# Optimization experiments

Measured on AMD Instinct MI355X. Metric: run time of the kernel, lower is better.

Reference implementation:

```python
import jax, jax.numpy as jnp
import numpy as np

THRESHOLD = 0.05

def binarize101(w, threshold):
    # Ternary quantization to {-1, 0, +1}: zero inside the dead-zone [-thr, thr].
    pos = (w > threshold).astype(w.dtype)
    neg = (w < -threshold).astype(w.dtype)
    return pos - neg

def setup_inputs() -> dict:
    key = jax.random.key(0)
    k1, k2, k3 = jax.random.split(key, 3)
    x = jax.random.normal(k1, (8192, 4096), dtype=jnp.float32)
    weight = jax.random.normal(k2, (4096, 4096), dtype=jnp.float32)
    bias = jax.random.normal(k3, (4096,), dtype=jnp.float32)
    return {"x": x, "weight": weight, "bias": bias}

def reference(x, weight, bias):
    wb = binarize101(weight, THRESHOLD)
    # F.linear: x @ wb.T + bias ; x: [N, in], weight: [out, in] -> [N, out]
    return jnp.einsum('ni,oi->no', x, wb) + bias
```

## Files before the change

kernel.cpp:

```cpp
#include <hip/hip_runtime.h>

typedef float floatx16 __attribute__((ext_vector_type(16)));
typedef __bf16 bf16x8 __attribute__((ext_vector_type(8)));
using u16 = unsigned short;
using u32 = unsigned int;

#define GLOBAL_AS __attribute__((address_space(1)))
#define LDS_AS    __attribute__((address_space(3)))

__device__ __forceinline__ u32 rne_bf16(float f) {
  u32 u = __float_as_uint(f);
  return (u + 0x7FFFu + ((u >> 16) & 1u)) >> 16;
}

__global__ __launch_bounds__(256) void cvt_x_perm(const float* __restrict__ x,
                                                  u16* __restrict__ xb, int K) {
  __shared__ u16 sm[16384];
  const int tid = threadIdx.x;
  const int Kt = K >> 6;
  const int pn = blockIdx.x / Kt, tt = blockIdx.x % Kt;
  const float* src = x + (size_t)pn * 256 * K + tt * 64;
#pragma unroll
  for (int j = 0; j < 16; ++j) {
    const int fc = j * 256 + tid;
    const int row = fc >> 4, kl4 = fc & 15;
    const float4 v = *(const float4*)(src + (size_t)row * K + kl4 * 4);
    uint2 o;
    o.x = rne_bf16(v.x) | (rne_bf16(v.y) << 16);
    o.y = rne_bf16(v.z) | (rne_bf16(v.w) << 16);
    const int gi = row >> 5, rowin = row & 31;
    const int ks = kl4 >> 2;
    const int lane = rowin + 32 * ((kl4 >> 1) & 1);
    const int e4 = (kl4 & 1) * 4;
    *(uint2*)(sm + gi * 2048 + ks * 512 + lane * 8 + e4) = o;
  }
  __syncthreads();
  u16* dst = xb + (size_t)pn * 256 * K + (size_t)tt * 16384;
#pragma unroll
  for (int j = 0; j < 8; ++j) {
    const int o = (j * 256 + tid) * 8;
    *(uint4*)(dst + o) = *(const uint4*)(sm + o);
  }
}

__global__ __launch_bounds__(256) void quant_w_perm(const float* __restrict__ w,
                                                    u16* __restrict__ wb, int K) {
  __shared__ u16 sm[16384];
  const int tid = threadIdx.x;
  const int Kt = K >> 6;
  const int pn = blockIdx.x / Kt, tt = blockIdx.x % Kt;
  const float* src = w + (size_t)pn * 256 * K + tt * 64;
#pragma unroll
  for (int j = 0; j < 16; ++j) {
    const int fc = j * 256 + tid;
    const int row = fc >> 4, kl4 = fc & 15;
    const float4 v = *(const float4*)(src + (size_t)row * K + kl4 * 4);
    float vv[4] = {v.x, v.y, v.z, v.w};
    u32 r[4];
#pragma unroll
    for (int e = 0; e < 4; ++e)
      r[e] = (vv[e] > 0.05f) ? 0x3F80u : ((vv[e] < -0.05f) ? 0xBF80u : 0u);
    uint2 o;
    o.x = r[0] | (r[1] << 16);
    o.y = r[2] | (r[3] << 16);
    const int gi = row >> 5, rowin = row & 31;
    const int ks = kl4 >> 2;
    const int lane = rowin + 32 * ((kl4 >> 1) & 1);
    const int e4 = (kl4 & 1) * 4;
    *(uint2*)(sm + gi * 2048 + ks * 512 + lane * 8 + e4) = o;
  }
  __syncthreads();
  u16* dst = wb + (size_t)pn * 256 * K + (size_t)tt * 16384;
#pragma unroll
  for (int j = 0; j < 8; ++j) {
    const int o = (j * 256 + tid) * 8;
    *(uint4*)(dst + o) = *(const uint4*)(sm + o);
  }
}

__global__ __launch_bounds__(512, 2) void gemm_bin_flow(
    const u16* __restrict__ Ap, const u16* __restrict__ Bp,
    const float* __restrict__ bias, float* __restrict__ C,
    int M, int N, int K) {
  __shared__ u16 lds[65536];

  const int tid = threadIdx.x;
  const int w = tid >> 6, l = tid & 63;
  const int wr = w >> 2, wc = w & 3;

  const int nbn = N >> 8;
  int wg = blockIdx.x;
  const int nwg = gridDim.x;
  if ((nwg & 7) == 0) wg = (wg & 7) * (nwg >> 3) + (wg >> 3);
  const int bm = wg / nbn, bn = wg % nbn;

  const int T = K >> 6;

  const u16* const Abase = Ap + (size_t)bm * ((size_t)K << 8) + tid * 8;
  const u16* const Bbase = Bp + (size_t)bn * ((size_t)K << 8) + tid * 8;

  const u16* const afp0 = lds + wr * 8192 + l * 8;
  const u16* const bfp0 = lds + 16384 + wc * 4096 + l * 8;

  floatx16 acc[4][2] = {};
  bf16x8 af[8], af2[8], bflo[4], bfhi[4];

#define GLOAD(gptr, u16off)                                                    \
  __builtin_amdgcn_global_load_lds((const GLOBAL_AS void*)(gptr),              \
                                   (LDS_AS void*)(lds + (u16off)), 16, 0, 0)
#define STAGE8(tt, bufdst)                                                     \
  {                                                                            \
    const size_t tb_ = (size_t)(tt) * 16384;                                   \
    GLOAD(Abase + tb_ + 0 * 4096, (bufdst) + 0 + tid * 8);                     \
    GLOAD(Abase + tb_ + 1 * 4096, (bufdst) + 4096 + tid * 8);                  \
    GLOAD(Abase + tb_ + 2 * 4096, (bufdst) + 8192 + tid * 8);                  \
    GLOAD(Abase + tb_ + 3 * 4096, (bufdst) + 12288 + tid * 8);                 \
    GLOAD(Bbase + tb_ + 0 * 4096, (bufdst) + 16384 + tid * 8);                 \
    GLOAD(Bbase + tb_ + 1 * 4096, (bufdst) + 20480 + tid * 8);                 \
    GLOAD(Bbase + tb_ + 2 * 4096, (bufdst) + 24576 + tid * 8);                 \
    GLOAD(Bbase + tb_ + 3 * 4096, (bufdst) + 28672 + tid * 8);                 \
  }

  STAGE8(0, 0)
  asm volatile("s_waitcnt vmcnt(0)" ::: "memory");
  __builtin_amdgcn_s_barrier();

  for (int t = 0; t < T; ++t) {
    const int bufc = (t & 1) << 15;
    const int bufo = bufc ^ 32768;
    const bool st1 = (t + 1 < T);

    if (st1) STAGE8(t + 1, bufo)

    const u16* afp = afp0 + bufc;
    const u16* bfp = bfp0 + bufc;

#pragma unroll
    for (int m = 0; m < 2; ++m)
#pragma unroll
      for (int ks = 0; ks < 4; ++ks)
        af[m * 4 + ks] = *(const bf16x8*)(afp + m * 2048 + ks * 512);
#pragma unroll
    for (int ks = 0; ks < 4; ++ks) bflo[ks] = *(const bf16x8*)(bfp + ks * 512);
#pragma unroll
    for (int ks = 0; ks < 4; ++ks) bfhi[ks] = *(const bf16x8*)(bfp + 2048 + ks * 512);

    asm volatile("s_waitcnt lgkmcnt(4)" ::: "memory");
    __builtin_amdgcn_sched_barrier(0);
    __builtin_amdgcn_s_setprio(1);
#pragma unroll
    for (int ks = 0; ks < 4; ++ks)
#pragma unroll
      for (int m = 0; m < 2; ++m)
        acc[m][0] = __builtin_amdgcn_mfma_f32_32x32x16_bf16(
            af[m * 4 + ks], bflo[ks], acc[m][0], 0, 0, 0);
    __builtin_amdgcn_s_setprio(0);

#pragma unroll
    for (int m = 0; m < 2; ++m)
#pragma unroll
      for (int ks = 0; ks < 4; ++ks)
        af2[m * 4 + ks] = *(const bf16x8*)(afp + 4096 + m * 2048 + ks * 512);

    asm volatile("s_waitcnt lgkmcnt(8)" ::: "memory");
    __builtin_amdgcn_sched_barrier(0);
    __builtin_amdgcn_s_setprio(1);
#pragma unroll
    for (int ks = 0; ks < 4; ++ks)
#pragma unroll
      for (int m = 0; m < 2; ++m)
        acc[m][1] = __builtin_amdgcn_mfma_f32_32x32x16_bf16(
            af[m * 4 + ks], bfhi[ks], acc[m][1], 0, 0, 0);
    __builtin_amdgcn_s_setprio(0);

    asm volatile("s_waitcnt lgkmcnt(0)" ::: "memory");
    __builtin_amdgcn_sched_barrier(0);
    __builtin_amdgcn_s_setprio(1);
#pragma unroll
    for (int ks = 0; ks < 4; ++ks)
#pragma unroll
      for (int m = 0; m < 2; ++m)
        acc[2 + m][0] = __builtin_amdgcn_mfma_f32_32x32x16_bf16(
            af2[m * 4 + ks], bflo[ks], acc[2 + m][0], 0, 0, 0);
#pragma unroll
    for (int ks = 0; ks < 4; ++ks)
#pragma unroll
      for (int m = 0; m < 2; ++m)
        acc[2 + m][1] = __builtin_amdgcn_mfma_f32_32x32x16_bf16(
            af2[m * 4 + ks], bfhi[ks], acc[2 + m][1], 0, 0, 0);
    __builtin_amdgcn_s_setprio(0);

    if (st1) {
      asm volatile("s_waitcnt vmcnt(0)" ::: "memory");
      __builtin_amdgcn_s_barrier();
    }
  }
#undef STAGE8
#undef GLOAD

  const int colq = l & 31;
  const int hi4 = (l >> 5) * 4;
#pragma unroll
  for (int m = 0; m < 4; ++m) {
    const int rowb = bm * 256 + wr * 128 + m * 32 + hi4;
#pragma unroll
    for (int n = 0; n < 2; ++n) {
      const int col = bn * 256 + wc * 64 + n * 32 + colq;
      const float bv = bias[col];
      float* cp = C + (size_t)rowb * N + col;
#pragma unroll
      for (int q = 0; q < 16; ++q) {
        const int dr = (q & 3) + 8 * (q >> 2);
        cp[(size_t)dr * N] = acc[m][n][q] + bv;
      }
    }
  }
}

__global__ void gemm_naive_kernel(const float* __restrict__ x, const float* __restrict__ wgt,
                                  const float* __restrict__ bias, float* __restrict__ out,
                                  int M, int N, int K) {
  long long idx = (long long)blockIdx.x * blockDim.x + threadIdx.x;
  if (idx >= (long long)M * N) return;
  int o = (int)(idx % N);
  int m = (int)(idx / N);
  const float* xr = x + (size_t)m * K;
  const float* wr = wgt + (size_t)o * K;
  float s = 0.f;
  for (int i = 0; i < K; ++i) {
    float wv = wr[i];
    float t = (wv > 0.05f) ? 1.f : ((wv < -0.05f) ? -1.f : 0.f);
    s = fmaf(xr[i], t, s);
  }
  out[idx] = s + bias[o];
}

extern "C" void kernel_launch(void* const* d_in, const int* in_sizes, int n_in,
                              void* d_out, int out_size, void* d_ws, size_t ws_size,
                              hipStream_t stream) {
  const float* x    = (const float*)d_in[0];
  const float* wgt  = (const float*)d_in[1];
  const float* bias = (const float*)d_in[2];
  float* out = (float*)d_out;

  const int N = in_sizes[2];
  const int K = in_sizes[1] / N;
  const int M = in_sizes[0] / K;

  const size_t need = ((size_t)M * K + (size_t)N * K) * sizeof(u16);
  if (ws_size >= need && (M % 256 == 0) && (N % 256 == 0) && (K % 64 == 0) && K >= 192) {
    u16* xb = (u16*)d_ws;
    u16* wb = xb + (size_t)M * K;
    const int Kt = K / 64;
    cvt_x_perm<<<(M / 256) * Kt, 256, 0, stream>>>(x, xb, K);
    quant_w_perm<<<(N / 256) * Kt, 256, 0, stream>>>(wgt, wb, K);
    const int grid = (M / 256) * (N / 256);
    gemm_bin_flow<<<grid, 512, 0, stream>>>(xb, wb, bias, out, M, N, K);
  } else {
    const long long total = (long long)M * N;
    gemm_naive_kernel<<<(unsigned)((total + 255) / 256), 256, 0, stream>>>(x, wgt, bias, out, M, N, K);
  }
}
```

Measured before the change: 290.5 us.

## Pack ternary weights to 2 bits and decode B fragments in registers

The weight quantizer now writes each ternary value as a 2-bit code, packed in a fragment-ordered layout, so the GEMM loads B straight from global memory into registers and decodes it to bf16 there. The B tile no longer goes through LDS, which halves LDS use, cuts B global traffic by 8x, and frees registers by reusing one A fragment array. The A staging is reorganised into split half-tile loads overlapped with compute using a two-tile-ahead schedule and an extra barrier. The costs are ALU work for decoding inside the main loop, uncoalesced 2-byte scattered writes in the pack kernel, and a stricter K requirement (multiple of 128).

Result: slower. 359.4 us (+23.7%).

```diff
diff --git a/kernel.cpp b/kernel.cpp
--- a/kernel.cpp
+++ b/kernel.cpp
@@ -43,46 +43,46 @@
   }
 }
 
-__global__ __launch_bounds__(256) void quant_w_perm(const float* __restrict__ w,
-                                                    u16* __restrict__ wb, int K) {
-  __shared__ u16 sm[16384];
-  const int tid = threadIdx.x;
+__global__ void quant_w_pack(const float* __restrict__ w, u16* __restrict__ wb,
+                             int K, int Kd8, int n8) {
+  int stride = gridDim.x * blockDim.x;
   const int Kt = K >> 6;
-  const int pn = blockIdx.x / Kt, tt = blockIdx.x % Kt;
-  const float* src = w + (size_t)pn * 256 * K + tt * 64;
-#pragma unroll
-  for (int j = 0; j < 16; ++j) {
-    const int fc = j * 256 + tid;
-    const int row = fc >> 4, kl4 = fc & 15;
-    const float4 v = *(const float4*)(src + (size_t)row * K + kl4 * 4);
-    float vv[4] = {v.x, v.y, v.z, v.w};
-    u32 r[4];
-#pragma unroll
-    for (int e = 0; e < 4; ++e)
-      r[e] = (vv[e] > 0.05f) ? 0x3F80u : ((vv[e] < -0.05f) ? 0xBF80u : 0u);
-    uint2 o;
-    o.x = r[0] | (r[1] << 16);
-    o.y = r[2] | (r[3] << 16);
-    const int gi = row >> 5, rowin = row & 31;
-    const int ks = kl4 >> 2;
-    const int lane = rowin + 32 * ((kl4 >> 1) & 1);
-    const int e4 = (kl4 & 1) * 4;
-    *(uint2*)(sm + gi * 2048 + ks * 512 + lane * 8 + e4) = o;
-  }
-  __syncthreads();
-  u16* dst = wb + (size_t)pn * 256 * K + (size_t)tt * 16384;
-#pragma unroll
-  for (int j = 0; j < 8; ++j) {
-    const int o = (j * 256 + tid) * 8;
-    *(uint4*)(dst + o) = *(const uint4*)(sm + o);
-  }
-}
-
-__global__ __launch_bounds__(512, 2) void gemm_bin_flow(
+  for (int i = blockIdx.x * blockDim.x + threadIdx.x; i < n8; i += stride) {
+    const int n = i / Kd8;
+    const int k = (i - n * Kd8) * 8;
+    const float4* p = (const float4*)(w + (size_t)n * K + k);
+    float4 a = p[0], b = p[1];
+    float v[8] = {a.x, a.y, a.z, a.w, b.x, b.y, b.z, b.w};
+    u32 pk = 0;
+#pragma unroll
+    for (int j = 0; j < 8; ++j) {
+      u32 c = (v[j] > 0.05f) ? 1u : ((v[j] < -0.05f) ? 3u : 0u);
+      pk |= c << (2 * j);
+    }
+    const int bnp = n >> 8, wc = (n >> 6) & 3, ng = (n >> 5) & 1, cc = n & 31;
+    const int t = k >> 6, ks = (k >> 4) & 3, h = (k >> 3) & 1;
+    const int f = ng * 4 + ks, l = cc + 32 * h;
+    wb[(size_t)((bnp * Kt + t) * 4 + wc) * 512 + l * 8 + f] = (u16)pk;
+  }
+}
+
+__device__ __forceinline__ bf16x8 dec_frag(u32 pkv) {
+  union { u32 w[4]; bf16x8 v; } u;
+#pragma unroll
+  for (int ii = 0; ii < 4; ++ii) {
+    u32 x = (pkv >> (4 * ii)) & 0xFu;
+    u32 lo = (x & 1u) * 0x3F80u | ((x & 2u) << 14);
+    u32 hi = ((x >> 2) & 1u) * 0x3F80u | ((x & 8u) << 12);
+    u.w[ii] = lo | (hi << 16);
+  }
+  return u.v;
+}
+
+__global__ __launch_bounds__(512, 2) void gemm_bin_breg(
     const u16* __restrict__ Ap, const u16* __restrict__ Bp,
     const float* __restrict__ bias, float* __restrict__ C,
     int M, int N, int K) {
-  __shared__ u16 lds[65536];
+  __shared__ u16 lds[32768];
 
   const int tid = threadIdx.x;
   const int w = tid >> 6, l = tid & 63;
@@ -95,107 +95,116 @@
   const int bm = wg / nbn, bn = wg % nbn;
 
   const int T = K >> 6;
+  const int Kt = T;
 
   const u16* const Abase = Ap + (size_t)bm * ((size_t)K << 8) + tid * 8;
-  const u16* const Bbase = Bp + (size_t)bn * ((size_t)K << 8) + tid * 8;
+  const u16* const pkp = Bp + (size_t)((size_t)bn * Kt * 4 + wc) * 512 + l * 8;
 
   const u16* const afp0 = lds + wr * 8192 + l * 8;
-  const u16* const bfp0 = lds + 16384 + wc * 4096 + l * 8;
 
   floatx16 acc[4][2] = {};
-  bf16x8 af[8], af2[8], bflo[4], bfhi[4];
+  bf16x8 af[8], bflo[4], bfhi[4];
+  uint4 pkA, pkB;
 
 #define GLOAD(gptr, u16off)                                                    \
   __builtin_amdgcn_global_load_lds((const GLOBAL_AS void*)(gptr),              \
                                    (LDS_AS void*)(lds + (u16off)), 16, 0, 0)
-#define STAGE8(tt, bufdst)                                                     \
+
+  pkA = *(const uint4*)(pkp);
+  GLOAD(Abase + 0 * 4096,      0 + tid * 8);
+  GLOAD(Abase + 1 * 4096,   4096 + tid * 8);
+  GLOAD(Abase + 2 * 4096,   8192 + tid * 8);
+  GLOAD(Abase + 3 * 4096,  12288 + tid * 8);
+  if (T > 1) {
+    GLOAD(Abase + 16384 + 0 * 4096, 16384 + 0 + tid * 8);
+    GLOAD(Abase + 16384 + 2 * 4096, 16384 + 8192 + tid * 8);
+    pkB = *(const uint4*)(pkp + 2048);
+  }
+  asm volatile("s_waitcnt vmcnt(3)" ::: "memory");
+  __builtin_amdgcn_s_barrier();
+
+#define TILE(t, PKX)                                                           \
   {                                                                            \
-    const size_t tb_ = (size_t)(tt) * 16384;                                   \
-    GLOAD(Abase + tb_ + 0 * 4096, (bufdst) + 0 + tid * 8);                     \
-    GLOAD(Abase + tb_ + 1 * 4096, (bufdst) + 4096 + tid * 8);                  \
-    GLOAD(Abase + tb_ + 2 * 4096, (bufdst) + 8192 + tid * 8);                  \
-    GLOAD(Abase + tb_ + 3 * 4096, (bufdst) + 12288 + tid * 8);                 \
-    GLOAD(Bbase + tb_ + 0 * 4096, (bufdst) + 16384 + tid * 8);                 \
-    GLOAD(Bbase + tb_ + 1 * 4096, (bufdst) + 20480 + tid * 8);                 \
-    GLOAD(Bbase + tb_ + 2 * 4096, (bufdst) + 24576 + tid * 8);                 \
-    GLOAD(Bbase + tb_ + 3 * 4096, (bufdst) + 28672 + tid * 8);                 \
-  }
-
-  STAGE8(0, 0)
-  asm volatile("s_waitcnt vmcnt(0)" ::: "memory");
-  __builtin_amdgcn_s_barrier();
-
-  for (int t = 0; t < T; ++t) {
-    const int bufc = (t & 1) << 15;
-    const int bufo = bufc ^ 32768;
-    const bool st1 = (t + 1 < T);
-
-    if (st1) STAGE8(t + 1, bufo)
-
-    const u16* afp = afp0 + bufc;
-    const u16* bfp = bfp0 + bufc;
-
-#pragma unroll
-    for (int m = 0; m < 2; ++m)
-#pragma unroll
-      for (int ks = 0; ks < 4; ++ks)
-        af[m * 4 + ks] = *(const bf16x8*)(afp + m * 2048 + ks * 512);
-#pragma unroll
-    for (int ks = 0; ks < 4; ++ks) bflo[ks] = *(const bf16x8*)(bfp + ks * 512);
-#pragma unroll
-    for (int ks = 0; ks < 4; ++ks) bfhi[ks] = *(const bf16x8*)(bfp + 2048 + ks * 512);
-
-    asm volatile("s_waitcnt lgkmcnt(4)" ::: "memory");
-    __builtin_amdgcn_sched_barrier(0);
-    __builtin_amdgcn_s_setprio(1);
-#pragma unroll
-    for (int ks = 0; ks < 4; ++ks)
-#pragma unroll
-      for (int m = 0; m < 2; ++m)
-        acc[m][0] = __builtin_amdgcn_mfma_f32_32x32x16_bf16(
-            af[m * 4 + ks], bflo[ks], acc[m][0], 0, 0, 0);
-    __builtin_amdgcn_s_setprio(0);
-
-#pragma unroll
-    for (int m = 0; m < 2; ++m)
-#pragma unroll
-      for (int ks = 0; ks < 4; ++ks)
-        af2[m * 4 + ks] = *(const bf16x8*)(afp + 4096 + m * 2048 + ks * 512);
-
-    asm volatile("s_waitcnt lgkmcnt(8)" ::: "memory");
-    __builtin_amdgcn_sched_barrier(0);
-    __builtin_amdgcn_s_setprio(1);
-#pragma unroll
-    for (int ks = 0; ks < 4; ++ks)
-#pragma unroll
-      for (int m = 0; m < 2; ++m)
-        acc[m][1] = __builtin_amdgcn_mfma_f32_32x32x16_bf16(
-            af[m * 4 + ks], bfhi[ks], acc[m][1], 0, 0, 0);
-    __builtin_amdgcn_s_setprio(0);
-
-    asm volatile("s_waitcnt lgkmcnt(0)" ::: "memory");
-    __builtin_amdgcn_sched_barrier(0);
-    __builtin_amdgcn_s_setprio(1);
-#pragma unroll
-    for (int ks = 0; ks < 4; ++ks)
-#pragma unroll
-      for (int m = 0; m < 2; ++m)
-        acc[2 + m][0] = __builtin_amdgcn_mfma_f32_32x32x16_bf16(
-            af2[m * 4 + ks], bflo[ks], acc[2 + m][0], 0, 0, 0);
-#pragma unroll
-    for (int ks = 0; ks < 4; ++ks)
-#pragma unroll
-      for (int m = 0; m < 2; ++m)
-        acc[2 + m][1] = __builtin_amdgcn_mfma_f32_32x32x16_bf16(
-            af2[m * 4 + ks], bfhi[ks], acc[2 + m][1], 0, 0, 0);
-    __builtin_amdgcn_s_setprio(0);
-
-    if (st1) {
-      asm volatile("s_waitcnt vmcnt(0)" ::: "memory");
-      __builtin_amdgcn_s_barrier();
-    }
-  }
-#undef STAGE8
+    const int bufc = ((t) & 1) << 14;                                          \
+    const int bufo = bufc ^ 16384;                                             \
+    const bool st1 = (t) + 1 < T;                                              \
+    const bool st2 = (t) + 2 < T;                                              \
+    const u16* afp = afp0 + bufc;                                              \
+           \
+    _Pragma("unroll")                                                          \
+    for (int m = 0; m < 2; ++m)                                                \
+      _Pragma("unroll")                                                        \
+      for (int ks = 0; ks < 4; ++ks)                                           \
+        af[m * 4 + ks] = *(const bf16x8*)(afp + m * 2048 + ks * 512);          \
+    if (st1) {                                                                 \
+      const size_t tb_ = (size_t)((t) + 1) * 16384;                            \
+      GLOAD(Abase + tb_ + 1 * 4096, bufo + 4096 + tid * 8);                    \
+      GLOAD(Abase + tb_ + 3 * 4096, bufo + 12288 + tid * 8);                   \
+    }                                                                          \
+    _Pragma("unroll")                                                          \
+    for (int ks = 0; ks < 4; ++ks) bflo[ks] = dec_frag((ks & 1) ? (((const u32*)&PKX)[ks >> 1] >> 16) : (((const u32*)&PKX)[ks >> 1] & 0xFFFFu)); \
+    asm volatile("s_waitcnt lgkmcnt(0)" ::: "memory");                         \
+    __builtin_amdgcn_sched_barrier(0);                                         \
+    __builtin_amdgcn_s_barrier();         \
+    __builtin_amdgcn_s_setprio(1);                                             \
+    _Pragma("unroll")                                                          \
+    for (int ks = 0; ks < 4; ++ks)                                             \
+      _Pragma("unroll")                                                        \
+      for (int m = 0; m < 2; ++m)                                              \
+        acc[m][0] = __builtin_amdgcn_mfma_f32_32x32x16_bf16(                   \
+            af[m * 4 + ks], bflo[ks], acc[m][0], 0, 0, 0);                     \
+    __builtin_amdgcn_s_setprio(0);                                             \
+                         \
+    if (st2) {                                                                 \
+      const size_t tb_ = (size_t)((t) + 2) * 16384;                            \
+      GLOAD(Abase + tb_ + 0 * 4096, bufc + 0 + tid * 8);                       \
+      GLOAD(Abase + tb_ + 2 * 4096, bufc + 8192 + tid * 8);                    \
+    }                                                                          \
+    _Pragma("unroll")                                                          \
+    for (int ks = 0; ks < 4; ++ks) bfhi[ks] = dec_frag((ks & 1) ? (((const u32*)&PKX)[2 + (ks >> 1)] >> 16) : (((const u32*)&PKX)[2 + (ks >> 1)] & 0xFFFFu)); \
+    __builtin_amdgcn_s_setprio(1);                                             \
+    _Pragma("unroll")                                                          \
+    for (int ks = 0; ks < 4; ++ks)                                             \
+      _Pragma("unroll")                                                        \
+      for (int m = 0; m < 2; ++m)                                              \
+        acc[m][1] = __builtin_amdgcn_mfma_f32_32x32x16_bf16(                   \
+            af[m * 4 + ks], bfhi[ks], acc[m][1], 0, 0, 0);                     \
+    __builtin_amdgcn_s_setprio(0);                                             \
+                                                  \
+    _Pragma("unroll")                                                          \
+    for (int m = 0; m < 2; ++m)                                                \
+      _Pragma("unroll")                                                        \
+      for (int ks = 0; ks < 4; ++ks)                                           \
+        af[m * 4 + ks] = *(const bf16x8*)(afp + 4096 + m * 2048 + ks * 512);   \
+    if (st2) PKX = *(const uint4*)(pkp + (size_t)((t) + 2) * 2048);            \
+    asm volatile("s_waitcnt lgkmcnt(0)" ::: "memory");                         \
+    __builtin_amdgcn_sched_barrier(0);                                         \
+    __builtin_amdgcn_s_setprio(1);                                             \
+    _Pragma("unroll")                                                          \
+    for (int ks = 0; ks < 4; ++ks)                                             \
+      _Pragma("unroll")                                                        \
+      for (int m = 0; m < 2; ++m)                                              \
+        acc[2 + m][0] = __builtin_amdgcn_mfma_f32_32x32x16_bf16(               \
+            af[m * 4 + ks], bflo[ks], acc[2 + m][0], 0, 0, 0);                 \
+    _Pragma("unroll")                                                          \
+    for (int ks = 0; ks < 4; ++ks)                                             \
+      _Pragma("unroll")                                                        \
+      for (int m = 0; m < 2; ++m)                                              \
+        acc[2 + m][1] = __builtin_amdgcn_mfma_f32_32x32x16_bf16(               \
+            af[m * 4 + ks], bfhi[ks], acc[2 + m][1], 0, 0, 0);                 \
+    __builtin_amdgcn_s_setprio(0);                                             \
+    if (st1) {                                                                 \
+      if (st2) asm volatile("s_waitcnt vmcnt(3)" ::: "memory");                \
+      else     asm volatile("s_waitcnt vmcnt(0)" ::: "memory");                \
+      __builtin_amdgcn_s_barrier();         \
+    }                                                                          \
+  }
+
+  for (int tt = 0; tt < T; tt += 2) {
+    TILE(tt,     pkA)
+    TILE(tt + 1, pkB)
+  }
+#undef TILE
 #undef GLOAD
 
   const int colq = l & 31;
@@ -247,15 +256,15 @@
   const int K = in_sizes[1] / N;
   const int M = in_sizes[0] / K;
 
-  const size_t need = ((size_t)M * K + (size_t)N * K) * sizeof(u16);
-  if (ws_size >= need && (M % 256 == 0) && (N % 256 == 0) && (K % 64 == 0) && K >= 192) {
+  const size_t need = (size_t)M * K * 2 + (size_t)N * K / 4;
+  if (ws_size >= need && (M % 256 == 0) && (N % 256 == 0) && (K % 128 == 0) && K >= 256) {
     u16* xb = (u16*)d_ws;
     u16* wb = xb + (size_t)M * K;
     const int Kt = K / 64;
     cvt_x_perm<<<(M / 256) * Kt, 256, 0, stream>>>(x, xb, K);
-    quant_w_perm<<<(N / 256) * Kt, 256, 0, stream>>>(wgt, wb, K);
+    quant_w_pack<<<2048, 256, 0, stream>>>(wgt, wb, K, K / 8, (N * K) / 8);
     const int grid = (M / 256) * (N / 256);
-    gemm_bin_flow<<<grid, 512, 0, stream>>>(xb, wb, bias, out, M, N, K);
+    gemm_bin_breg<<<grid, 512, 0, stream>>>(xb, wb, bias, out, M, N, K);
   } else {
     const long long total = (long long)M * N;
     gemm_naive_kernel<<<(unsigned)((total + 255) / 256), 256, 0, stream>>>(x, wgt, bias, out, M, N, K);
```
